# Performance work log

Measured on AMD Instinct MI355X. Metric: run time of the kernel, lower is better.

The kernel has to match this reference:

```python
import jax, jax.numpy as jnp
import numpy as np


def setup_inputs() -> dict:
    key = jax.random.key(0)
    k1, k2 = jax.random.split(key)
    B, N1, N2 = 4, 8192, 8192
    pc1 = jax.random.normal(k1, (B, N1, 3), dtype=jnp.float32)
    pc2 = jax.random.normal(k2, (B, N2, 3), dtype=jnp.float32)
    return {"pc1": pc1, "pc2": pc2}


def reference(pc1, pc2):
    """Chamfer distance: CD(P,Q) = mean_p min_q ||p-q||^2 + mean_q min_p ||q-p||^2.

    pc1: (B, N1, 3), pc2: (B, N2, 3) -> (B,)
    Uses ||p-q||^2 = ||p||^2 + ||q||^2 - 2 p.q to avoid the (B,N1,N2,3)
    broadcasted-difference intermediate; only the (B,N1,N2) matrix is formed.
    """
    sq1 = jnp.sum(pc1 * pc1, axis=-1)                     # (B, N1)
    sq2 = jnp.sum(pc2 * pc2, axis=-1)                     # (B, N2)
    cross = jnp.einsum("bnd,bmd->bnm", pc1, pc2)          # (B, N1, N2)
    dist = sq1[:, :, None] + sq2[:, None, :] - 2.0 * cross  # (B, N1, N2)
    d12 = jnp.min(dist, axis=2).mean(axis=1)              # (B,) pc1 -> pc2
    d21 = jnp.min(dist, axis=1).mean(axis=1)              # (B,) pc2 -> pc1
    return d12 + d21
```

## Files before the change

kernel.cpp:

```cpp
#include <hip/hip_runtime.h>


typedef _Float16 half8  __attribute__((ext_vector_type(8)));
typedef float    f32x16 __attribute__((ext_vector_type(16)));

#define NPTS   8192
#define NB     4
#define SPLITS 8
#define TPW    32
#define QWIN   (TPW * 32)

#define MFMA_Z(d, a, b)                                                \
    asm("v_mfma_f32_32x32x16_f16 %0, %1, %2, 0"                        \
        : "=&v"(d) : "v"(a), "v"(b))

#define MIN3(dst, s0, s1)                                              \
    asm("v_min3_f32 %0, %1, %2, %0"                                    \
        : "+v"(dst) : "v"(s0), "v"(s1))

#define SB() __builtin_amdgcn_sched_barrier(0)

#define STEP2(q0, q1)                                                  \
    do {                                                               \
        {                                                              \
            f32x16 acc0, acc1;                                         \
            MFMA_Z(acc0, a0, q0);                                      \
            MFMA_Z(acc1, a0, q1);                                      \
            SB();                                                      \
            asm volatile("s_nop 7\n\ts_nop 7\n\ts_nop 3");             \
            SB();                                                      \
            _Pragma("unroll")                                          \
            for (int r = 0; r < 16; ++r) MIN3(rm0[r], acc0[r], acc1[r]); \
            SB();                                                      \
        }                                                              \
        {                                                              \
            f32x16 acc0, acc1;                                         \
            MFMA_Z(acc0, a1, q0);                                      \
            MFMA_Z(acc1, a1, q1);                                      \
            SB();                                                      \
            asm volatile("s_nop 7\n\ts_nop 7\n\ts_nop 3");             \
            SB();                                                      \
            _Pragma("unroll")                                          \
            for (int r = 0; r < 16; ++r) MIN3(rm1[r], acc0[r], acc1[r]); \
            SB();                                                      \
        }                                                              \
    } while (0)

__global__ __launch_bounds__(256) void chamfer_main(
    const float* __restrict__ pc1, const float* __restrict__ pc2,
    float* __restrict__ ws_row)
{
    __shared__ half8 Bf[(TPW + 2) * 64];

    int bid = blockIdx.x;
    const int pt  = bid & 31;            bid >>= 5;
    const int qs  = bid & (SPLITS - 1);  bid >>= 3;
    const int b   = bid & (NB - 1);      bid >>= 2;
    const int dir = bid;

    const int tid = threadIdx.x;
    const int w = tid >> 6, lane = tid & 63;
    const int col = lane & 31, g = lane >> 5;
    const int pbase = pt * 256 + w * 64;

    const float* Acl = dir ? pc2 : pc1;
    const float* Bcl = dir ? pc1 : pc2;

    const _Float16 one = (_Float16)1.0f, zz = (_Float16)0.0f;

    for (int i = tid; i < QWIN; i += 256) {
        const int t = i >> 5, c = i & 31;
        const float* Q = Bcl + ((size_t)b * NPTS + qs * QWIN + i) * 3;
        const float qx = Q[0], qy = Q[1], qz = Q[2];

        const _Float16 hx = (_Float16)qx, hy = (_Float16)qy, hz = (_Float16)qz;
        const _Float16 lx = (_Float16)(qx - (float)hx);
        const _Float16 ly = (_Float16)(qy - (float)hy);
        const _Float16 lz = (_Float16)(qz - (float)hz);
        const float sq = fmaf(qx, qx, fmaf(qy, qy, qz * qz));
        const _Float16 sh = (_Float16)sq;
        const _Float16 sl = (_Float16)(sq - (float)sh);

        const _Float16 nhx = (_Float16)(-2.0f * (float)hx);
        const _Float16 nhy = (_Float16)(-2.0f * (float)hy);
        const _Float16 nhz = (_Float16)(-2.0f * (float)hz);
        const _Float16 nlx = (_Float16)(-2.0f * (float)lx);
        const _Float16 nly = (_Float16)(-2.0f * (float)ly);
        const _Float16 nlz = (_Float16)(-2.0f * (float)lz);

        Bf[t * 64 + c]      = (half8){nhx, nhy, nhz, nlx, nly, nlz, nhx, nhy};
        Bf[t * 64 + 32 + c] = (half8){nhz, one, one, sh,  sl,  zz,  zz,  zz};
    }

    half8 a0, a1;
    #pragma unroll
    for (int h = 0; h < 2; ++h) {
        const float* P = Acl + ((size_t)b * NPTS + pbase + h * 32 + col) * 3;
        const float px = P[0], py = P[1], pz = P[2];
        const _Float16 hx = (_Float16)px, hy = (_Float16)py, hz = (_Float16)pz;
        const _Float16 lx = (_Float16)(px - (float)hx);
        const _Float16 ly = (_Float16)(py - (float)hy);
        const _Float16 lz = (_Float16)(pz - (float)hz);
        const float sq1 = fmaf(px, px, fmaf(py, py, pz * pz));
        const _Float16 sh = (_Float16)sq1;
        const _Float16 sl = (_Float16)(sq1 - (float)sh);
        half8 a;
        if (g == 0) a = (half8){hx, hy, hz, hx, hy, hz, lx, ly};
        else        a = (half8){lz, sh, sl, one, one, zz, zz, zz};
        if (h == 0) a0 = a; else a1 = a;
    }

    float rm0[16], rm1[16];
    #pragma unroll
    for (int r = 0; r < 16; ++r) { rm0[r] = 3.402823466e+38f;
                                   rm1[r] = 3.402823466e+38f; }

    __syncthreads();

    half8 pA0 = Bf[0 * 64 + lane], pA1 = Bf[1 * 64 + lane];
    half8 pB0, pB1;

    for (int t = 0; t < TPW; t += 4) {
        pB0 = Bf[(t + 2) * 64 + lane];
        pB1 = Bf[(t + 3) * 64 + lane];
        STEP2(pA0, pA1);
        pA0 = Bf[(t + 4) * 64 + lane];
        pA1 = Bf[(t + 5) * 64 + lane];
        STEP2(pB0, pB1);
    }

    __syncthreads();
    float* RB = (float*)Bf;
    #pragma unroll
    for (int r = 0; r < 16; ++r) {
        RB[((w * 2 + 0) * 16 + r) * 64 + lane] = rm0[r];
        RB[((w * 2 + 1) * 16 + r) * 64 + lane] = rm1[r];
    }
    __syncthreads();

    {
        const int ww = tid >> 6, h = (tid >> 5) & 1, R = tid & 31;
        const int r  = (R & 3) + 4 * (R >> 3);
        const int gg = (R >> 2) & 1;
        const float* src = RB + (((ww * 2 + h) * 16 + r) * 64 + gg * 32);
        float m0 = fminf(src[0], src[1]);
        #pragma unroll
        for (int k = 2; k < 32; k += 2)
            m0 = fminf(m0, fminf(src[k], src[k + 1]));
        const size_t obase = (((size_t)dir * NB + b) * SPLITS + qs) * NPTS
                             + (size_t)pt * 256;
        ws_row[obase + ww * 64 + h * 32 + R] = m0;
    }
}

__global__ __launch_bounds__(256) void chamfer_reduce(
    const float* __restrict__ ws_row, float* __restrict__ partial)
{
    int bid = blockIdx.x;
    const int sl  = bid & 31; bid >>= 5;
    const int b   = bid & 3;  bid >>= 2;
    const int dir = bid;

    const int p = sl * 256 + threadIdx.x;
    const float* base = ws_row + (((size_t)dir * NB + b) * SPLITS) * NPTS + p;
    float m0 = fminf(base[0],        base[NPTS]);
    float m1 = fminf(base[2 * NPTS], base[3 * NPTS]);
    float m2 = fminf(base[4 * NPTS], base[5 * NPTS]);
    float m3 = fminf(base[6 * NPTS], base[7 * NPTS]);
    float sum = fminf(fminf(m0, m1), fminf(m2, m3));

    for (int off = 32; off; off >>= 1) sum += __shfl_down(sum, off, 64);
    __shared__ float red[4];
    if (!(threadIdx.x & 63)) red[threadIdx.x >> 6] = sum;
    __syncthreads();
    if (!threadIdx.x)
        partial[blockIdx.x] = red[0] + red[1] + red[2] + red[3];
}

__global__ __launch_bounds__(64) void chamfer_final(
    const float* __restrict__ partial, float* __restrict__ out)
{
    const int b = blockIdx.x, t = threadIdx.x;
    const int dir = t >> 5, sl = t & 31;
    float v = partial[(((size_t)dir * NB + b) << 5) + sl];
    for (int off = 32; off; off >>= 1) v += __shfl_down(v, off, 64);
    if (!t) out[b] = v * (1.0f / (float)NPTS);
}

extern "C" void kernel_launch(void* const* d_in, const int* in_sizes, int n_in,
                              void* d_out, int out_size, void* d_ws, size_t ws_size,
                              hipStream_t stream)
{
    const float* pc1 = (const float*)d_in[0];
    const float* pc2 = (const float*)d_in[1];
    float* out = (float*)d_out;

    char* ws = (char*)d_ws;
    float* ws_row  = (float*)ws;
    float* partial = (float*)(ws + (2 << 20));

    chamfer_main<<<2048, 256, 0, stream>>>(pc1, pc2, ws_row);
    chamfer_reduce<<<256, 256, 0, stream>>>(ws_row, partial);
    chamfer_final<<<NB, 64, 0, stream>>>(partial, out);
}
```

Before: 27.76 us.

## Software-pipeline MFMA and min3 reduction with rotating accumulator pairs

Restructures the inner loop so that while one pair of MFMA results is computing, the min3 reduction consumes the previous pair's accumulators. This replaces the explicit s_nop stalls between each MFMA and its dependent min3 with useful work, leaving only a prologue nop. It uses twice as many live accumulator registers, which raises VGPR pressure and relies on the MFMA latency being covered by 16 min3 instructions.

```diff
diff --git a/kernel.cpp b/kernel.cpp
--- a/kernel.cpp
+++ b/kernel.cpp
@@ -20,30 +20,20 @@
 
 #define SB() __builtin_amdgcn_sched_barrier(0)
 
-#define STEP2(q0, q1)                                                  \
+#define PAIR_ROT(q0, q1)                                               \
     do {                                                               \
-        {                                                              \
-            f32x16 acc0, acc1;                                         \
-            MFMA_Z(acc0, a0, q0);                                      \
-            MFMA_Z(acc1, a0, q1);                                      \
-            SB();                                                      \
-            asm volatile("s_nop 7\n\ts_nop 7\n\ts_nop 3");             \
-            SB();                                                      \
-            _Pragma("unroll")                                          \
-            for (int r = 0; r < 16; ++r) MIN3(rm0[r], acc0[r], acc1[r]); \
-            SB();                                                      \
-        }                                                              \
-        {                                                              \
-            f32x16 acc0, acc1;                                         \
-            MFMA_Z(acc0, a1, q0);                                      \
-            MFMA_Z(acc1, a1, q1);                                      \
-            SB();                                                      \
-            asm volatile("s_nop 7\n\ts_nop 7\n\ts_nop 3");             \
-            SB();                                                      \
-            _Pragma("unroll")                                          \
-            for (int r = 0; r < 16; ++r) MIN3(rm1[r], acc0[r], acc1[r]); \
-            SB();                                                      \
-        }                                                              \
+        MFMA_Z(x0, a0, q0);                                            \
+        MFMA_Z(x1, a0, q1);                                            \
+        SB();                                                          \
+        _Pragma("unroll")                                              \
+        for (int r = 0; r < 16; ++r) MIN3(rm1[r], y0[r], y1[r]);       \
+        SB();                                                          \
+        MFMA_Z(y0, a1, q0);                                            \
+        MFMA_Z(y1, a1, q1);                                            \
+        SB();                                                          \
+        _Pragma("unroll")                                              \
+        for (int r = 0; r < 16; ++r) MIN3(rm0[r], x0[r], x1[r]);       \
+        SB();                                                          \
     } while (0)
 
 __global__ __launch_bounds__(256) void chamfer_main(
@@ -118,16 +108,35 @@
     __syncthreads();
 
     half8 pA0 = Bf[0 * 64 + lane], pA1 = Bf[1 * 64 + lane];
-    half8 pB0, pB1;
-
-    for (int t = 0; t < TPW; t += 4) {
-        pB0 = Bf[(t + 2) * 64 + lane];
-        pB1 = Bf[(t + 3) * 64 + lane];
-        STEP2(pA0, pA1);
-        pA0 = Bf[(t + 4) * 64 + lane];
-        pA1 = Bf[(t + 5) * 64 + lane];
-        STEP2(pB0, pB1);
-    }
+    half8 pB0 = Bf[2 * 64 + lane], pB1 = Bf[3 * 64 + lane];
+    f32x16 x0, x1, y0, y1;
+
+    MFMA_Z(x0, a0, pA0);
+    MFMA_Z(x1, a0, pA1);
+    SB();
+    asm volatile("s_nop 7\n\ts_nop 7\n\ts_nop 3");
+    SB();
+    MFMA_Z(y0, a1, pA0);
+    MFMA_Z(y1, a1, pA1);
+    SB();
+    #pragma unroll
+    for (int r = 0; r < 16; ++r) MIN3(rm0[r], x0[r], x1[r]);
+    SB();
+    pA0 = Bf[4 * 64 + lane];
+    pA1 = Bf[5 * 64 + lane];
+
+    for (int j = 0; j < 7; ++j) {
+        PAIR_ROT(pB0, pB1);
+        pB0 = Bf[(6 + 4 * j) * 64 + lane];
+        pB1 = Bf[(7 + 4 * j) * 64 + lane];
+        PAIR_ROT(pA0, pA1);
+        pA0 = Bf[(8 + 4 * j) * 64 + lane];
+        pA1 = Bf[(9 + 4 * j) * 64 + lane];
+    }
+
+    PAIR_ROT(pB0, pB1);
+    #pragma unroll
+    for (int r = 0; r < 16; ++r) MIN3(rm1[r], y0[r], y1[r]);
 
     __syncthreads();
     float* RB = (float*)Bf;
```

Result: faster. 27.03 us, median of 2 (-2.6%).
